# Kernel optimization log

Hardware: AMD Instinct MI355X
Metric: run time of the kernel (lower is better)

The kernel has to match this reference:

```python
import jax, jax.numpy as jnp
import numpy as np

EPS_BN = 1e-5
EPS_SIM = 1e-8
PAD = 1
NUM_ITERS = 3


def capsule_conv2d(x, w):
    # x: [B, C, H, W]; w: [out_caps, in_caps, kh, kw, in_len, out_len]
    B, C, H, W = x.shape
    oc, ic, kh, kw, il, ol = w.shape
    # im2col patches, feature dim ordered (c, kh, kw) -> matches torch.unfold
    patches = jax.lax.conv_general_dilated_patches(
        x, (kh, kw), (1, 1), [(PAD, PAD), (PAD, PAD)])  # [B, C*kh*kw, H, W]
    N = H * W
    p = patches.reshape(B, ic, il, kh * kw, N)
    p = jnp.transpose(p, (0, 4, 1, 3, 2))  # [B, N, ic, kk, il]
    wf = w.reshape(oc, ic, kh * kw, il, ol)
    # per-patch capsule transform -> priors [B, N, oc, ic*kk, ol]
    priors = jnp.einsum('bnikl,oiklm->bnoikm', p, wf)
    priors = priors.reshape(B, N, oc, ic * kh * kw, ol)
    # k-means routing with Tonimoto similarity, 3 iterations, no squash
    out = priors.mean(axis=-2, keepdims=True)  # [B, N, oc, 1, ol]
    for _ in range(NUM_ITERS):
        dot = jnp.sum(priors * out, axis=-1, keepdims=True)
        n1 = jnp.sum(priors * priors, axis=-1, keepdims=True)
        n2 = jnp.sum(out * out, axis=-1, keepdims=True)
        logits = dot / jnp.maximum(n1 + n2 - dot, EPS_SIM)
        probs = jax.nn.softmax(logits, axis=-2)
        out = jnp.sum(probs * priors, axis=-2, keepdims=True)
    out = out[..., 0, :]                      # [B, N, oc, ol]
    out = out.reshape(B, H, W, oc * ol)       # channels = oc*ol
    return jnp.transpose(out, (0, 3, 1, 2))   # [B, C, H, W]


def batchnorm2d(x, gamma, beta):
    mean = x.mean(axis=(0, 2, 3), keepdims=True)
    var = x.var(axis=(0, 2, 3), keepdims=True)  # biased, as torch BN training fwd
    inv = jax.lax.rsqrt(var + EPS_BN)
    return gamma[None, :, None, None] * (x - mean) * inv + beta[None, :, None, None]


def setup_inputs() -> dict:
    key = jax.random.key(0)
    k0, k1, k2 = jax.random.split(key, 3)
    B, C, H, W = 2, 64, 96, 96
    IL = OL = 8
    x = jax.random.normal(k0, (B, C, H, W), jnp.float32)
    w1 = jax.random.normal(k1, (C // OL, C // IL, 3, 3, IL, OL), jnp.float32) * 0.1
    w2 = jax.random.normal(k2, (C // OL, C // OL, 3, 3, OL, OL), jnp.float32) * 0.1
    g1 = jnp.ones((C,), jnp.float32)
    b1 = jnp.zeros((C,), jnp.float32)
    g2 = jnp.ones((C,), jnp.float32)
    b2 = jnp.zeros((C,), jnp.float32)
    return {"x": x, "w1": w1, "g1": g1, "b1": b1, "w2": w2, "g2": g2, "b2": b2}


def reference(x, w1, g1, b1, w2, g2, b2):
    r = batchnorm2d(capsule_conv2d(x, w1), g1, b1)
    r = batchnorm2d(capsule_conv2d(r, w2), g2, b2)
    return x + r
```

## Files before the change

### kernel.cpp

```cpp
#include <hip/hip_runtime.h>
#include <hip/hip_bf16.h>

#define HW 9216
#define NPC 18432
#define NELEM 1179648
#define XSTR 72
#define PATCH_B 7776
#define XREC 12
#define XBUF_B (4*2*16*2*XREC*4)

typedef __attribute__((ext_vector_type(2))) float f32x2;
typedef __attribute__((ext_vector_type(4))) float f32x4v;
typedef __attribute__((ext_vector_type(8))) short short8v;

__device__ __forceinline__ int detect_is32(const unsigned short* __restrict__ w1u) {
    int lane = threadIdx.x & 63;
    int bad = 0;
    #pragma unroll
    for (int i = 0; i < 16; ++i) {
        unsigned short u = (unsigned short)(w1u[lane + i * 64] & 0x7FFF);
        bad |= (u >= 0x42C8);
    }
    return (__ballot(bad) != 0ULL) ? 1 : 0;
}

__device__ __forceinline__ float load_in(const void* p, int idx, int is32) {
    return is32 ? ((const float*)p)[idx]
                : __bfloat162float(((const __hip_bfloat16*)p)[idx]);
}

__device__ __forceinline__ float lo16(unsigned v) { return __int_as_float((int)(v << 16)); }
__device__ __forceinline__ float hi16(unsigned v) { return __int_as_float((int)(v & 0xFFFF0000u)); }
__device__ __forceinline__ unsigned pk2bf(float a, float b) {
    __hip_bfloat162 h = __float22bfloat162_rn(float2{a, b});
    return *(unsigned*)&h;
}

__launch_bounds__(256)
__global__ void prep_kernel(const void* __restrict__ x,
                            const void* __restrict__ w1, const void* __restrict__ w2,
                            __hip_bfloat16* __restrict__ xt,
                            __hip_bfloat16* __restrict__ Bfr1,
                            __hip_bfloat16* __restrict__ Bfr2,
                            float* __restrict__ statz) {
    __shared__ float tile[64 * 33];
    const int bid = blockIdx.x;
    if (bid < 576) {
        const int is32 = detect_is32((const unsigned short*)w1);
        int xb = bid % 3, y = (bid / 3) % 96, b = bid / 288;
        int x0 = xb * 32;
        for (int e = threadIdx.x; e < 2048; e += 256) {
            int xl = e & 31, c = e >> 5;
            tile[c * 33 + xl] = load_in(x, ((b * 64 + c) * 96 + y) * 96 + x0 + xl, is32);
        }
        __syncthreads();
        for (int f = threadIdx.x; f < 1024; f += 256) {
            int c2 = f & 31, xl = f >> 5;
            float a = tile[(2 * c2) * 33 + xl];
            float c = tile[(2 * c2 + 1) * 33 + xl];
            *(unsigned*)&xt[((b * 96 + y) * 96 + x0 + xl) * 64 + 2 * c2] = pk2bf(a, c);
        }
    } else if (bid < 720) {
        const int is32 = detect_is32((const unsigned short*)w1);
        int t = (bid - 576) * 256 + threadIdx.x;
        int layer = t / 18432;
        int r = t - layer * 18432;
        int lane = r & 63;
        int fi = r >> 6;
        int h = fi & 1, g = (fi >> 1) & 1;
        int kq = fi >> 2;
        int k = kq % 9, o = kq / 9;
        int dy = k / 3, dx = k % 3;
        int quad = lane >> 4, colhi = (lane >> 3) & 1, m = lane & 7;
        int act = (quad == 2 * h + colhi);
        int i = g * 4 + 2 * h + colhi;
        const void* w = layer ? w2 : w1;
        __hip_bfloat16* dst = layer ? Bfr2 : Bfr1;
        #pragma unroll
        for (int j = 0; j < 8; ++j) {
            float v = act ? load_in(w, ((((o * 8 + i) * 3 + dy) * 3 + dx) * 8 + j) * 8 + m, is32)
                          : 0.f;
            dst[(fi * 64 + lane) * 8 + j] = __float2bfloat16(v);
        }
    } else {
        for (int e = threadIdx.x; e < 2048; e += 256) statz[e] = 0.f;
    }
}

__device__ __forceinline__ void xexchange(float* __restrict__ xbufF, int slot,
                                          int o2w, int pos16, int g, int quad,
                                          int mhalf, float ac[4], float& se) {
    float* rec = xbufF + ((((slot * 2 + o2w) * 16 + pos16) * 2 + g) * XREC);
    if (quad < 2) {
        *(float4*)(rec + quad * 4) = make_float4(ac[0], ac[1], ac[2], ac[3]);
        if (quad == 0) rec[8] = se;
    }
    __syncthreads();
    const float* prec = xbufF + ((((slot * 2 + o2w) * 16 + pos16) * 2 + (1 - g)) * XREC);
    float4 po = *(const float4*)(prec + mhalf * 4);
    ac[0] += po.x; ac[1] += po.y; ac[2] += po.z; ac[3] += po.w;
    se += prec[8];
}

__launch_bounds__(256, 4)
__global__ void caps_kernel(const __hip_bfloat16* __restrict__ in,
                            const float* __restrict__ statPrev,
                            const void* __restrict__ gamma, const void* __restrict__ beta,
                            const void* __restrict__ wdt,
                            const __hip_bfloat16* __restrict__ Bfr,
                            __hip_bfloat16* __restrict__ yout,
                            float* __restrict__ statL,
                            int layer1) {
    __shared__ __align__(16) unsigned char smem[PATCH_B + XBUF_B];
    __hip_bfloat16* patchH = (__hip_bfloat16*)smem;
    float* xbufF = (float*)(smem + PATCH_B);
    float* omF = (float*)smem;
    float* scL = (float*)(smem + PATCH_B);
    float* shL = scL + 64;

    const int gx    = blockIdx.x;
    const int opair = gx & 3;
    const int x0    = (gx >> 2) * 16;
    const int y  = blockIdx.y;
    const int b  = blockIdx.z;
    const int tid = threadIdx.x;

    if (!layer1) {
        if (tid < 64) {
            const int is32 = detect_is32((const unsigned short*)wdt);
            int c = tid;
            float s = 0.f, ss = 0.f;
            #pragma unroll
            for (int cp = 0; cp < 8; ++cp) {
                s  += statPrev[cp * 128 + c];
                ss += statPrev[cp * 128 + 64 + c];
            }
            float mean = s * (1.f / (float)NPC);
            float var  = fmaxf(ss * (1.f / (float)NPC) - mean * mean, 0.f);
            float inv  = rsqrtf(var + 1e-5f);
            float g = load_in(gamma, c, is32) * inv;
            scL[c] = g;
            shL[c] = load_in(beta, c, is32) - mean * g;
        }
        __syncthreads();
    }

    for (int e = tid; e < 864; e += 256) {
        int c4 = e & 15;
        int q  = e >> 4;
        int xo = q % 18, row = q / 18;
        int yy = y + row - 1, xx = x0 + xo - 1;
        uint2 v = {0u, 0u};
        if (yy >= 0 && yy < 96 && xx >= 0 && xx < 96) {
            v = *(const uint2*)&in[((b * 96 + yy) * 96 + xx) * 64 + c4 * 4];
            if (!layer1) {
                int c = c4 * 4;
                float f0 = lo16(v.x) * scL[c]     + shL[c];
                float f1 = hi16(v.x) * scL[c + 1] + shL[c + 1];
                float f2 = lo16(v.y) * scL[c + 2] + shL[c + 2];
                float f3 = hi16(v.y) * scL[c + 3] + shL[c + 3];
                v.x = pk2bf(f0, f1);
                v.y = pk2bf(f2, f3);
            }
        }
        *(uint2*)&patchH[q * XSTR + c4 * 4] = v;
    }
    __syncthreads();

    const int lane  = tid & 63;
    const int wv    = tid >> 6;
    const int o2w   = wv >> 1;
    const int g     = wv & 1;
    const int pos16 = lane & 15;
    const int quad  = lane >> 4;
    const int mhalf = quad & 1;

    f32x4v P[9][2];
    {
        const int o = opair * 2 + o2w;
        #pragma unroll
        for (int k = 0; k < 9; ++k) {
            const int dy = k / 3, dx = k % 3;
            short8v a = *(const short8v*)&patchH[(dy * 18 + dx + pos16) * XSTR + g * 32 + quad * 8];
            #pragma unroll
            for (int h = 0; h < 2; ++h) {
                short8v bf = *(const short8v*)&Bfr[((((o * 9 + k) * 2 + g) * 2 + h) * 64 + lane) * 8];
                P[k][h] = __builtin_amdgcn_mfma_f32_16x16x32_bf16(bf, a, (f32x4v){0.f, 0.f, 0.f, 0.f}, 0, 0, 0);
            }
        }
    }

    float n1o[9];
    #pragma unroll
    for (int k = 0; k < 9; ++k) {
        float np0 = P[k][0][0] * P[k][0][0];
        np0 = fmaf(P[k][0][1], P[k][0][1], np0);
        np0 = fmaf(P[k][0][2], P[k][0][2], np0);
        np0 = fmaf(P[k][0][3], P[k][0][3], np0);
        float np1 = P[k][1][0] * P[k][1][0];
        np1 = fmaf(P[k][1][1], P[k][1][1], np1);
        np1 = fmaf(P[k][1][2], P[k][1][2], np1);
        np1 = fmaf(P[k][1][3], P[k][1][3], np1);
        float own = mhalf ? np1 : np0;
        float oth = mhalf ? np0 : np1;
        n1o[k] = own + __shfl_xor(oth, 16, 64);
    }

    float om[4];
    {
        float ac[4];
        #pragma unroll
        for (int r = 0; r < 4; ++r) {
            float s = 0.f;
            #pragma unroll
            for (int k = 0; k < 9; ++k) s += P[k][0][r] + P[k][1][r];
            s += __shfl_xor(s, 32, 64);
            ac[r] = s;
        }
        float dummy = 0.f;
        xexchange(xbufF, 0, o2w, pos16, g, quad, mhalf, ac, dummy);
        #pragma unroll
        for (int r = 0; r < 4; ++r) om[r] = ac[r] * (1.f / 72.f);
    }
    float n2;
    {
        float n2p = om[0] * om[0];
        n2p = fmaf(om[1], om[1], n2p);
        n2p = fmaf(om[2], om[2], n2p);
        n2p = fmaf(om[3], om[3], n2p);
        n2 = n2p + __shfl_xor(n2p, 16, 64);
    }

    #pragma unroll
    for (int it = 0; it < 3; ++it) {
        float se = 0.f;
        float ac[4] = {0.f, 0.f, 0.f, 0.f};
        #pragma unroll
        for (int k = 0; k < 9; ++k) {
            float dp0 = P[k][0][0] * om[0];
            dp0 = fmaf(P[k][0][1], om[1], dp0);
            dp0 = fmaf(P[k][0][2], om[2], dp0);
            dp0 = fmaf(P[k][0][3], om[3], dp0);
            float dp1 = P[k][1][0] * om[0];
            dp1 = fmaf(P[k][1][1], om[1], dp1);
            dp1 = fmaf(P[k][1][2], om[2], dp1);
            dp1 = fmaf(P[k][1][3], om[3], dp1);
            float own = mhalf ? dp1 : dp0;
            float oth = mhalf ? dp0 : dp1;
            float d = own + __shfl_xor(oth, 16, 64);
            float denom = fmaxf(n1o[k] + n2 - d, 1e-8f);
            float e = __expf(d * __builtin_amdgcn_rcpf(denom));
            se += e;
            float e_oth = __shfl_xor(e, 16, 64);
            float eh0 = mhalf ? e_oth : e;
            float eh1 = mhalf ? e : e_oth;
            ac[0] = fmaf(eh0, P[k][0][0], fmaf(eh1, P[k][1][0], ac[0]));
            ac[1] = fmaf(eh0, P[k][0][1], fmaf(eh1, P[k][1][1], ac[1]));
            ac[2] = fmaf(eh0, P[k][0][2], fmaf(eh1, P[k][1][2], ac[2]));
            ac[3] = fmaf(eh0, P[k][0][3], fmaf(eh1, P[k][1][3], ac[3]));
        }
        se += __shfl_xor(se, 16, 64);
        se += __shfl_xor(se, 32, 64);
        #pragma unroll
        for (int r = 0; r < 4; ++r) ac[r] += __shfl_xor(ac[r], 32, 64);
        xexchange(xbufF, 1 + it, o2w, pos16, g, quad, mhalf, ac, se);
        float inv = __builtin_amdgcn_rcpf(se);
        #pragma unroll
        for (int r = 0; r < 4; ++r) om[r] = ac[r] * inv;
        float n2p = om[0] * om[0];
        n2p = fmaf(om[1], om[1], n2p);
        n2p = fmaf(om[2], om[2], n2p);
        n2p = fmaf(om[3], om[3], n2p);
        n2 = n2p + __shfl_xor(n2p, 16, 64);
    }

    if (g == 0 && quad < 2) {
        const int o = opair * 2 + o2w;
        uint2 pk;
        pk.x = pk2bf(om[0], om[1]);
        pk.y = pk2bf(om[2], om[3]);
        *(uint2*)&yout[((b * 96 + y) * 96 + x0 + pos16) * 64 + o * 8 + mhalf * 4] = pk;
        *(float4*)&omF[(o2w * 16 + pos16) * 8 + mhalf * 4] = make_float4(om[0], om[1], om[2], om[3]);
    }
    __syncthreads();

    if (tid < 32) {
        int c16 = tid & 15, sel = tid >> 4;
        int oo2 = c16 >> 3, m = c16 & 7;
        float v = 0.f;
        #pragma unroll
        for (int pp = 0; pp < 16; ++pp) {
            float t = omF[(oo2 * 16 + pp) * 8 + m];
            v += sel ? t * t : t;
        }
        int cp = (blockIdx.x + blockIdx.y * 3 + blockIdx.z) & 7;
        atomicAdd(&statL[cp * 128 + sel * 64 + (opair * 2 + oo2) * 8 + m], v);
    }
}

__launch_bounds__(256)
__global__ void final_kernel(const void* __restrict__ xin,
                             const __hip_bfloat16* __restrict__ yt2,
                             const float* __restrict__ statL,
                             const void* __restrict__ gamma, const void* __restrict__ beta,
                             const void* __restrict__ w1,
                             void* __restrict__ outp) {
    __shared__ float tile[64 * 33];
    __shared__ float scL[64], shL[64];
    const int is32 = detect_is32((const unsigned short*)w1);
    if (threadIdx.x < 64) {
        int c = threadIdx.x;
        float s = 0.f, ss = 0.f;
        #pragma unroll
        for (int cp = 0; cp < 8; ++cp) {
            s  += statL[cp * 128 + c];
            ss += statL[cp * 128 + 64 + c];
        }
        float mean = s * (1.f / (float)NPC);
        float var  = fmaxf(ss * (1.f / (float)NPC) - mean * mean, 0.f);
        float inv  = rsqrtf(var + 1e-5f);
        float g = load_in(gamma, c, is32) * inv;
        scL[c] = g;
        shL[c] = load_in(beta, c, is32) - mean * g;
    }
    __syncthreads();

    int x0 = blockIdx.x * 32, y = blockIdx.y, b = blockIdx.z;
    for (int e = threadIdx.x; e < 1024; e += 256) {
        int c2 = e & 31, xl = e >> 5;
        unsigned v = *(const unsigned*)&yt2[((b * 96 + y) * 96 + x0 + xl) * 64 + c2 * 2];
        int c = c2 * 2;
        tile[c * 33 + xl]       = lo16(v) * scL[c]     + shL[c];
        tile[(c + 1) * 33 + xl] = hi16(v) * scL[c + 1] + shL[c + 1];
    }
    __syncthreads();
    for (int f = threadIdx.x; f < 2048; f += 256) {
        int xl = f & 31, c = f >> 5;
        int idx = ((b * 64 + c) * 96 + y) * 96 + x0 + xl;
        float v = load_in(xin, idx, is32) + tile[c * 33 + xl];
        if (is32) ((float*)outp)[idx] = v;
        else      ((__hip_bfloat16*)outp)[idx] = __float2bfloat16(v);
    }
}

extern "C" void kernel_launch(void* const* d_in, const int* in_sizes, int n_in,
                              void* d_out, int out_size, void* d_ws, size_t ws_size,
                              hipStream_t stream) {
    const void* x  = d_in[0];
    const void* w1 = d_in[1];
    const void* g1 = d_in[2];
    const void* b1 = d_in[3];
    const void* w2 = d_in[4];
    const void* g2 = d_in[5];
    const void* b2 = d_in[6];

    __hip_bfloat16* bufA = (__hip_bfloat16*)d_ws;
    __hip_bfloat16* bufB = bufA + NELEM;
    __hip_bfloat16* Bfr1 = bufB + NELEM;
    __hip_bfloat16* Bfr2 = Bfr1 + 147456;
    float* statz = (float*)(Bfr2 + 147456);
    float* statL1 = statz;
    float* statL2 = statz + 1024;

    prep_kernel<<<721, 256, 0, stream>>>(x, w1, w2, bufA, Bfr1, Bfr2, statz);

    dim3 cgrid(24, 96, 2);
    caps_kernel<<<cgrid, 256, 0, stream>>>(bufA, nullptr, nullptr, nullptr, w1,
                                           Bfr1, bufB, statL1, 1);
    caps_kernel<<<cgrid, 256, 0, stream>>>(bufB, statL1, g1, b1, w1,
                                           Bfr2, bufA, statL2, 0);
    final_kernel<<<dim3(3, 96, 2), 256, 0, stream>>>(x, bufA, statL2, g2, b2, w1, d_out);
}
```

Measured before the change: 165.5 us.

## Park two prior tiles in LDS and permute weight fragments to drop selects

The weight-fragment layout is permuted per lane (h xor m>>2) so each lane's own half of the prior tile is always d0, which removes the mhalf select logic in the routing loop. The kernel now keeps only 7 of the 9 prior tile pairs in registers and parks the last two in a new 16 KB shared buffer, reloading them on every routing iteration. Norms and the mean sum are folded into the MFMA loop. The aim is to lower VGPR pressure and per-iteration ALU work, at the cost of more LDS traffic and a larger shared footprint that may cut how many blocks fit per CU.

```diff
diff --git a/kernel.cpp b/kernel.cpp
--- a/kernel.cpp
+++ b/kernel.cpp
@@ -6,6 +6,7 @@
 #define NELEM 1179648
 #define XSTR 72
 #define PATCH_B 7776
+#define PARK_B 16384
 #define XREC 12
 #define XBUF_B (4*2*16*2*XREC*4)
 
@@ -34,6 +35,21 @@
 __device__ __forceinline__ unsigned pk2bf(float a, float b) {
     __hip_bfloat162 h = __float22bfloat162_rn(float2{a, b});
     return *(unsigned*)&h;
+}
+
+__device__ __forceinline__ float dotsq4(const f32x4v a) {
+    float t = a[0] * a[0];
+    t = fmaf(a[1], a[1], t);
+    t = fmaf(a[2], a[2], t);
+    t = fmaf(a[3], a[3], t);
+    return t;
+}
+__device__ __forceinline__ float dot4(const f32x4v a, const float om[4]) {
+    float t = a[0] * om[0];
+    t = fmaf(a[1], om[1], t);
+    t = fmaf(a[2], om[2], t);
+    t = fmaf(a[3], om[3], t);
+    return t;
 }
 
 __launch_bounds__(256)
@@ -72,8 +88,9 @@
         int k = kq % 9, o = kq / 9;
         int dy = k / 3, dx = k % 3;
         int quad = lane >> 4, colhi = (lane >> 3) & 1, m = lane & 7;
-        int act = (quad == 2 * h + colhi);
-        int i = g * 4 + 2 * h + colhi;
+        int heff = h ^ (m >> 2);
+        int act = (quad == 2 * heff + colhi);
+        int i = g * 4 + 2 * heff + colhi;
         const void* w = layer ? w2 : w1;
         __hip_bfloat16* dst = layer ? Bfr2 : Bfr1;
         #pragma unroll
@@ -111,9 +128,10 @@
                             __hip_bfloat16* __restrict__ yout,
                             float* __restrict__ statL,
                             int layer1) {
-    __shared__ __align__(16) unsigned char smem[PATCH_B + XBUF_B];
+    __shared__ __align__(16) unsigned char smem[PATCH_B + PARK_B + XBUF_B];
     __hip_bfloat16* patchH = (__hip_bfloat16*)smem;
-    float* xbufF = (float*)(smem + PATCH_B);
+    float* parkF = (float*)(smem + PATCH_B);
+    float* xbufF = (float*)(smem + PATCH_B + PARK_B);
     float* omF = (float*)smem;
     float* scL = (float*)(smem + PATCH_B);
     float* shL = scL + 64;
@@ -175,48 +193,39 @@
     const int quad  = lane >> 4;
     const int mhalf = quad & 1;
 
-    f32x4v P[9][2];
+    f32x4v Q[7][2];
+    float n1o[9];
+    float s2[4] = {0.f, 0.f, 0.f, 0.f};
     {
         const int o = opair * 2 + o2w;
         #pragma unroll
         for (int k = 0; k < 9; ++k) {
             const int dy = k / 3, dx = k % 3;
             short8v a = *(const short8v*)&patchH[(dy * 18 + dx + pos16) * XSTR + g * 32 + quad * 8];
+            short8v bf0 = *(const short8v*)&Bfr[((((o * 9 + k) * 2 + g) * 2 + 0) * 64 + lane) * 8];
+            short8v bf1 = *(const short8v*)&Bfr[((((o * 9 + k) * 2 + g) * 2 + 1) * 64 + lane) * 8];
+            f32x4v d0 = __builtin_amdgcn_mfma_f32_16x16x32_bf16(bf0, a, (f32x4v){0.f, 0.f, 0.f, 0.f}, 0, 0, 0);
+            f32x4v d1 = __builtin_amdgcn_mfma_f32_16x16x32_bf16(bf1, a, (f32x4v){0.f, 0.f, 0.f, 0.f}, 0, 0, 0);
             #pragma unroll
-            for (int h = 0; h < 2; ++h) {
-                short8v bf = *(const short8v*)&Bfr[((((o * 9 + k) * 2 + g) * 2 + h) * 64 + lane) * 8];
-                P[k][h] = __builtin_amdgcn_mfma_f32_16x16x32_bf16(bf, a, (f32x4v){0.f, 0.f, 0.f, 0.f}, 0, 0, 0);
+            for (int r = 0; r < 4; ++r) s2[r] += d0[r] + d1[r];
+            float np1 = dotsq4(d1);
+            n1o[k] = dotsq4(d0) + __shfl_xor(np1, 16, 64);
+            if (k < 7) {
+                Q[k][0] = d0;
+                Q[k][1] = d1;
+            } else {
+                const int pb = (k - 7) * 2;
+                *(f32x4v*)(parkF + (pb    ) * 1024 + tid * 4) = d0;
+                *(f32x4v*)(parkF + (pb + 1) * 1024 + tid * 4) = d1;
             }
         }
-    }
-
-    float n1o[9];
-    #pragma unroll
-    for (int k = 0; k < 9; ++k) {
-        float np0 = P[k][0][0] * P[k][0][0];
-        np0 = fmaf(P[k][0][1], P[k][0][1], np0);
-        np0 = fmaf(P[k][0][2], P[k][0][2], np0);
-        np0 = fmaf(P[k][0][3], P[k][0][3], np0);
-        float np1 = P[k][1][0] * P[k][1][0];
-        np1 = fmaf(P[k][1][1], P[k][1][1], np1);
-        np1 = fmaf(P[k][1][2], P[k][1][2], np1);
-        np1 = fmaf(P[k][1][3], P[k][1][3], np1);
-        float own = mhalf ? np1 : np0;
-        float oth = mhalf ? np0 : np1;
-        n1o[k] = own + __shfl_xor(oth, 16, 64);
     }
 
     float om[4];
     {
         float ac[4];
         #pragma unroll
-        for (int r = 0; r < 4; ++r) {
-            float s = 0.f;
-            #pragma unroll
-            for (int k = 0; k < 9; ++k) s += P[k][0][r] + P[k][1][r];
-            s += __shfl_xor(s, 32, 64);
-            ac[r] = s;
-        }
+        for (int r = 0; r < 4; ++r) ac[r] = s2[r] + __shfl_xor(s2[r], 32, 64);
         float dummy = 0.f;
         xexchange(xbufF, 0, o2w, pos16, g, quad, mhalf, ac, dummy);
         #pragma unroll
@@ -224,10 +233,7 @@
     }
     float n2;
     {
-        float n2p = om[0] * om[0];
-        n2p = fmaf(om[1], om[1], n2p);
-        n2p = fmaf(om[2], om[2], n2p);
-        n2p = fmaf(om[3], om[3], n2p);
+        float n2p = dotsq4((f32x4v){om[0], om[1], om[2], om[3]});
         n2 = n2p + __shfl_xor(n2p, 16, 64);
     }
 
@@ -235,30 +241,31 @@
     for (int it = 0; it < 3; ++it) {
         float se = 0.f;
         float ac[4] = {0.f, 0.f, 0.f, 0.f};
-        #pragma unroll
-        for (int k = 0; k < 9; ++k) {
-            float dp0 = P[k][0][0] * om[0];
-            dp0 = fmaf(P[k][0][1], om[1], dp0);
-            dp0 = fmaf(P[k][0][2], om[2], dp0);
-            dp0 = fmaf(P[k][0][3], om[3], dp0);
-            float dp1 = P[k][1][0] * om[0];
-            dp1 = fmaf(P[k][1][1], om[1], dp1);
-            dp1 = fmaf(P[k][1][2], om[2], dp1);
-            dp1 = fmaf(P[k][1][3], om[3], dp1);
-            float own = mhalf ? dp1 : dp0;
-            float oth = mhalf ? dp0 : dp1;
-            float d = own + __shfl_xor(oth, 16, 64);
-            float denom = fmaxf(n1o[k] + n2 - d, 1e-8f);
-            float e = __expf(d * __builtin_amdgcn_rcpf(denom));
-            se += e;
-            float e_oth = __shfl_xor(e, 16, 64);
-            float eh0 = mhalf ? e_oth : e;
-            float eh1 = mhalf ? e : e_oth;
-            ac[0] = fmaf(eh0, P[k][0][0], fmaf(eh1, P[k][1][0], ac[0]));
-            ac[1] = fmaf(eh0, P[k][0][1], fmaf(eh1, P[k][1][1], ac[1]));
-            ac[2] = fmaf(eh0, P[k][0][2], fmaf(eh1, P[k][1][2], ac[2]));
-            ac[3] = fmaf(eh0, P[k][0][3], fmaf(eh1, P[k][1][3], ac[3]));
-        }
+        #define RBODY(q0, q1, n1k)                                             \
+        {                                                                      \
+            float dp0 = dot4(q0, om);                                          \
+            float dp1 = dot4(q1, om);                                          \
+            float d = dp0 + __shfl_xor(dp1, 16, 64);                           \
+            float denom = fmaxf((n1k) + n2 - d, 1e-8f);                        \
+            float e = __expf(d * __builtin_amdgcn_rcpf(denom));                \
+            se += e;                                                           \
+            float eo = __shfl_xor(e, 16, 64);                                  \
+            ac[0] = fmaf(e, (q0)[0], fmaf(eo, (q1)[0], ac[0]));                \
+            ac[1] = fmaf(e, (q0)[1], fmaf(eo, (q1)[1], ac[1]));                \
+            ac[2] = fmaf(e, (q0)[2], fmaf(eo, (q1)[2], ac[2]));                \
+            ac[3] = fmaf(e, (q0)[3], fmaf(eo, (q1)[3], ac[3]));                \
+        }
+        #pragma unroll
+        for (int k = 0; k < 7; ++k) RBODY(Q[k][0], Q[k][1], n1o[k]);
+        {
+            f32x4v p70 = *(const f32x4v*)(parkF + 0 * 1024 + tid * 4);
+            f32x4v p71 = *(const f32x4v*)(parkF + 1 * 1024 + tid * 4);
+            RBODY(p70, p71, n1o[7]);
+            f32x4v p80 = *(const f32x4v*)(parkF + 2 * 1024 + tid * 4);
+            f32x4v p81 = *(const f32x4v*)(parkF + 3 * 1024 + tid * 4);
+            RBODY(p80, p81, n1o[8]);
+        }
+        #undef RBODY
         se += __shfl_xor(se, 16, 64);
         se += __shfl_xor(se, 32, 64);
         #pragma unroll
@@ -267,10 +274,7 @@
         float inv = __builtin_amdgcn_rcpf(se);
         #pragma unroll
         for (int r = 0; r < 4; ++r) om[r] = ac[r] * inv;
-        float n2p = om[0] * om[0];
-        n2p = fmaf(om[1], om[1], n2p);
-        n2p = fmaf(om[2], om[2], n2p);
-        n2p = fmaf(om[3], om[3], n2p);
+        float n2p = dotsq4((f32x4v){om[0], om[1], om[2], om[3]});
         n2 = n2p + __shfl_xor(n2p, 16, 64);
     }
 
```

Measured after the change: 163.3 us. Within noise of the previous version (-1.3%).
